# Performance work log

Hardware: AMD Instinct MI355X
Metric: run time of the kernel (lower is better)

## Reference

```python
import jax, jax.numpy as jnp
import numpy as np

N_NODES = 100000

def _gcn_norm(edge_index, num_nodes):
    # add self-loops, compute symmetric normalization coeffs per edge
    loops = jnp.arange(num_nodes, dtype=edge_index.dtype)
    src = jnp.concatenate([edge_index[0], loops])
    dst = jnp.concatenate([edge_index[1], loops])
    deg = jax.ops.segment_sum(jnp.ones_like(dst, dtype=jnp.float32), dst,
                              num_segments=num_nodes)
    dinv = jnp.where(deg > 0, jax.lax.rsqrt(deg), 0.0)
    norm = dinv[src] * dinv[dst]  # [E + N]
    return src, dst, norm

def _gcn_conv(x, W, b, src, dst, norm, num_nodes):
    h = x @ W                              # [N, out] transform first (PyG order)
    msg = h[src] * norm[:, None]           # gather + scale
    out = jax.ops.segment_sum(msg, dst, num_segments=num_nodes)  # scatter-add
    return out + b

def setup_inputs() -> dict:
    key = jax.random.key(0)
    k1, k2, k3, k4 = jax.random.split(key, 4)
    F_in, H, C = 128, 64, 40
    x = jax.random.normal(k1, (N_NODES, F_in), dtype=jnp.float32)
    edge_index = jax.random.randint(k2, (2, 1600000), 0, N_NODES, dtype=jnp.int64)
    W1 = jax.random.normal(k3, (F_in, H), dtype=jnp.float32) / np.sqrt(F_in)
    b1 = jnp.zeros((H,), dtype=jnp.float32)
    W2 = jax.random.normal(k4, (H, C), dtype=jnp.float32) / np.sqrt(H)
    b2 = jnp.zeros((C,), dtype=jnp.float32)
    return {"x": x, "edge_index": edge_index, "W1": W1, "b1": b1, "W2": W2, "b2": b2}

def reference(x, edge_index, W1, b1, W2, b2):
    num_nodes = x.shape[0]
    src, dst, norm = _gcn_norm(edge_index, num_nodes)
    h = _gcn_conv(x, W1, b1, src, dst, norm, num_nodes)
    h = jax.nn.relu(h)
    # dropout is identity in eval mode (training=False)
    h = _gcn_conv(h, W2, b2, src, dst, norm, num_nodes)
    return jax.nn.log_softmax(h, axis=1)
```

## Files before the change

kernel.cpp:

```cpp
#include <hip/hip_runtime.h>
#include <math.h>

#define NPB 256
#define BSH 8
#define MAXNB 400
#define BIN_CHUNK 8192
#define HIST_CHUNK 16384

typedef __attribute__((ext_vector_type(8))) short bf16x8;
typedef __attribute__((ext_vector_type(4))) float f32x4;
typedef __attribute__((ext_vector_type(2))) float f32x2;

__device__ __forceinline__ unsigned short f2bf(float f){
  unsigned int u = __float_as_uint(f);
  unsigned int r = (u + 0x7FFFu + ((u >> 16) & 1u)) >> 16;
  return (unsigned short)r;
}

__device__ __forceinline__ bf16x8 cvt8(float4 a, float4 b){
  union { unsigned u[4]; bf16x8 v; } r;
  asm("v_cvt_pk_bf16_f32 %0, %1, %2" : "=v"(r.u[0]) : "v"(a.x), "v"(a.y));
  asm("v_cvt_pk_bf16_f32 %0, %1, %2" : "=v"(r.u[1]) : "v"(a.z), "v"(a.w));
  asm("v_cvt_pk_bf16_f32 %0, %1, %2" : "=v"(r.u[2]) : "v"(b.x), "v"(b.y));
  asm("v_cvt_pk_bf16_f32 %0, %1, %2" : "=v"(r.u[3]) : "v"(b.z), "v"(b.w));
  return r.v;
}

__global__ void k_prep(const float* __restrict__ W1, const float* __restrict__ W2,
                       unsigned short* __restrict__ w1t, unsigned short* __restrict__ w2t,
                       int* __restrict__ bcnt, int NB){
  int t = threadIdx.x;
  if(blockIdx.x == 0){
    for(int i = t; i < 8192; i += 256){
      int k = i >> 6, f = i & 63;
      w1t[f*128 + k] = f2bf(W1[i]);
    }
  } else {
    for(int i = t; i < 3072; i += 256){
      int c = i >> 6, k = i & 63;
      w2t[c*64 + k] = (c < 40) ? f2bf(W2[k*40 + c]) : (unsigned short)0;
    }
    for(int i = t; i < NB; i += 256) bcnt[i] = 0;
  }
}


__global__ __launch_bounds__(256) void k_bhist(const int* __restrict__ dst, int E,
                                               int* __restrict__ bcnt, int NB){
  __shared__ int l[MAXNB];
  int t = threadIdx.x;
  int base = blockIdx.x*HIST_CHUNK;
  int end = base + HIST_CHUNK; if(end > E) end = E;
  for(int b = t; b < NB; b += 256) l[b] = 0;
  __syncthreads();
  for(int i = base + t; i < end; i += 256) atomicAdd(&l[dst[i] >> BSH], 1);
  __syncthreads();
  for(int b = t; b < NB; b += 256){ int c = l[b]; if(c) atomicAdd(&bcnt[b], c); }
}

__global__ void k_bscan(const int* __restrict__ bcnt, int* __restrict__ bofs,
                        int* __restrict__ bcur, int NB, int E){
  __shared__ int sh[1024];
  int t = threadIdx.x;
  int c0 = (2*t   < NB) ? bcnt[2*t]   : 0;
  int c1 = (2*t+1 < NB) ? bcnt[2*t+1] : 0;
  sh[t] = c0 + c1; __syncthreads();
  for(int off = 1; off < 1024; off <<= 1){
    int v = (t >= off) ? sh[t - off] : 0;
    __syncthreads();
    sh[t] += v;
    __syncthreads();
  }
  int pairEx = sh[t] - (c0 + c1);
  if(2*t   < NB){ bofs[2*t]   = pairEx;      bcur[2*t]   = pairEx; }
  if(2*t+1 < NB){ bofs[2*t+1] = pairEx + c0; bcur[2*t+1] = pairEx + c0; }
  if(t == 0) bofs[NB] = E;
}

__global__ __launch_bounds__(256) void k_binpass(const int* __restrict__ src,
                          const int* __restrict__ dst, int E,
                          int* __restrict__ bcur, unsigned int* __restrict__ binned, int NB){
  __shared__ int lcnt[MAXNB];
  __shared__ int lpos[MAXNB];
  int t = threadIdx.x;
  int base = blockIdx.x * BIN_CHUNK;
  int end = base + BIN_CHUNK; if(end > E) end = E;
  for(int b = t; b < NB; b += 256) lcnt[b] = 0;
  __syncthreads();
  for(int i = base + t; i < end; i += 256)
    atomicAdd(&lcnt[dst[i] >> BSH], 1);
  __syncthreads();
  for(int b = t; b < NB; b += 256){
    int c = lcnt[b];
    lpos[b] = c ? atomicAdd(&bcur[b], c) : 0;
  }
  __syncthreads();
  for(int i = base + t; i < end; i += 256){
    int d = dst[i];
    int b = d >> BSH;
    unsigned int rec = (unsigned int)src[i] | ((unsigned int)(d & (NPB-1)) << 17);
    int p = atomicAdd(&lpos[b], 1);
    binned[p] = rec;
  }
}

__global__ __launch_bounds__(256) void k_bscatter(const unsigned int* __restrict__ binned,
     const int* __restrict__ bofs, int* __restrict__ csr, int* __restrict__ row_ofs,
     float* __restrict__ dinv, int N, int E, int NB){
  __shared__ int lcnt[NPB];
  __shared__ int lofs[NPB];
  __shared__ int lcur[NPB];
  __shared__ int wsum[4];
  int b = blockIdx.x, t = threadIdx.x;
  int beg = bofs[b], end = bofs[b+1];
  lcnt[t] = 0;
  __syncthreads();
  for(int i = beg + t; i < end; i += 256) atomicAdd(&lcnt[binned[i] >> 17], 1);
  __syncthreads();
  int c = lcnt[t];
  int lane = t & 63, wid = t >> 6;
  int v = c;
  #pragma unroll
  for(int off = 1; off < 64; off <<= 1){
    int nv = __shfl_up(v, off, 64);
    if(lane >= off) v += nv;
  }
  if(lane == 63) wsum[wid] = v;
  __syncthreads();
  int wpre = 0;
  #pragma unroll
  for(int k2 = 0; k2 < 4; k2++) if(k2 < wid) wpre += wsum[k2];
  int ex = wpre + v - c;
  lofs[t] = beg + ex; lcur[t] = 0;
  int node = (b << BSH) + t;
  if(node < N){
    row_ofs[node] = beg + ex;
    dinv[node] = rsqrtf((float)(c + 1));
  }
  __syncthreads();
  for(int i = beg + t; i < end; i += 256){
    unsigned int rec = binned[i];
    int dl = rec >> 17;
    int pos = lofs[dl] + atomicAdd(&lcur[dl], 1);
    csr[pos] = (int)(rec & 0x1FFFFu);
  }
  if(b == NB-1 && t == 0) row_ofs[N] = E;
}

__global__ __launch_bounds__(256) void k_gemm1(const float* __restrict__ x,
                        const unsigned short* __restrict__ w1t,
                        const float* __restrict__ dinv, unsigned int* __restrict__ g1, int n){
  __shared__ unsigned short xs[128*136];
  __shared__ unsigned short wt[64*136];
  int tid = threadIdx.x;
  int nodeBase = blockIdx.x*128;
  for(int i = tid; i < 1024; i += 256){
    int f = i >> 4, seg = i & 15;
    *(uint4*)&wt[f*136 + seg*8] = *(const uint4*)&w1t[f*128 + seg*8];
  }
  {
    const float4* x4 = (const float4*)x;
    for(int i = tid; i < 2048; i += 256){
      int node = i >> 4, seg = i & 15;
      float4 va = make_float4(0.f,0.f,0.f,0.f), vb = va;
      if(nodeBase + node < n){
        va = x4[(size_t)(nodeBase + node)*32 + seg*2];
        vb = x4[(size_t)(nodeBase + node)*32 + seg*2 + 1];
      }
      *(bf16x8*)&xs[node*136 + seg*8] = cvt8(va, vb);
    }
  }
  __syncthreads();

  int w = tid >> 6, lane = tid & 63;
  int ml = lane & 15, q = lane >> 4;
  int n0 = nodeBase + w*32 + ml;
  int n1 = n0 + 16;
  bool vn0 = n0 < n, vn1 = n1 < n;

  f32x4 a00 = {0.f,0.f,0.f,0.f}, a01 = {0.f,0.f,0.f,0.f},
        a02 = {0.f,0.f,0.f,0.f}, a03 = {0.f,0.f,0.f,0.f};
  f32x4 a10 = {0.f,0.f,0.f,0.f}, a11 = {0.f,0.f,0.f,0.f},
        a12 = {0.f,0.f,0.f,0.f}, a13 = {0.f,0.f,0.f,0.f};
  const unsigned short* brow = &xs[(w*32 + ml)*136 + q*8];
  const unsigned short* arow = &wt[ml*136 + q*8];
  #pragma unroll
  for(int s = 0; s < 4; s++){
    bf16x8 bb0 = *(const bf16x8*)(brow +        s*32);
    bf16x8 bb1 = *(const bf16x8*)(brow + 2176 + s*32);
    bf16x8 a0 = *(const bf16x8*)(arow +    0 + s*32);
    bf16x8 a1 = *(const bf16x8*)(arow + 2176 + s*32);
    bf16x8 a2 = *(const bf16x8*)(arow + 4352 + s*32);
    bf16x8 a3 = *(const bf16x8*)(arow + 6528 + s*32);
    a00 = __builtin_amdgcn_mfma_f32_16x16x32_bf16(a0, bb0, a00, 0, 0, 0);
    a01 = __builtin_amdgcn_mfma_f32_16x16x32_bf16(a1, bb0, a01, 0, 0, 0);
    a02 = __builtin_amdgcn_mfma_f32_16x16x32_bf16(a2, bb0, a02, 0, 0, 0);
    a03 = __builtin_amdgcn_mfma_f32_16x16x32_bf16(a3, bb0, a03, 0, 0, 0);
    a10 = __builtin_amdgcn_mfma_f32_16x16x32_bf16(a0, bb1, a10, 0, 0, 0);
    a11 = __builtin_amdgcn_mfma_f32_16x16x32_bf16(a1, bb1, a11, 0, 0, 0);
    a12 = __builtin_amdgcn_mfma_f32_16x16x32_bf16(a2, bb1, a12, 0, 0, 0);
    a13 = __builtin_amdgcn_mfma_f32_16x16x32_bf16(a3, bb1, a13, 0, 0, 0);
  }
  if(vn0){
    float dv = dinv[n0];
    unsigned base16 = ((unsigned)n0 << 4) + q;
    int p;
    p = __builtin_amdgcn_cvt_pk_fp8_f32(a00[0]*dv, a00[1]*dv, 0, false);
    p = __builtin_amdgcn_cvt_pk_fp8_f32(a00[2]*dv, a00[3]*dv, p, true);
    g1[base16 +  0] = (unsigned)p;
    p = __builtin_amdgcn_cvt_pk_fp8_f32(a01[0]*dv, a01[1]*dv, 0, false);
    p = __builtin_amdgcn_cvt_pk_fp8_f32(a01[2]*dv, a01[3]*dv, p, true);
    g1[base16 +  4] = (unsigned)p;
    p = __builtin_amdgcn_cvt_pk_fp8_f32(a02[0]*dv, a02[1]*dv, 0, false);
    p = __builtin_amdgcn_cvt_pk_fp8_f32(a02[2]*dv, a02[3]*dv, p, true);
    g1[base16 +  8] = (unsigned)p;
    p = __builtin_amdgcn_cvt_pk_fp8_f32(a03[0]*dv, a03[1]*dv, 0, false);
    p = __builtin_amdgcn_cvt_pk_fp8_f32(a03[2]*dv, a03[3]*dv, p, true);
    g1[base16 + 12] = (unsigned)p;
  }
  if(vn1){
    float dv = dinv[n1];
    unsigned base16 = ((unsigned)n1 << 4) + q;
    int p;
    p = __builtin_amdgcn_cvt_pk_fp8_f32(a10[0]*dv, a10[1]*dv, 0, false);
    p = __builtin_amdgcn_cvt_pk_fp8_f32(a10[2]*dv, a10[3]*dv, p, true);
    g1[base16 +  0] = (unsigned)p;
    p = __builtin_amdgcn_cvt_pk_fp8_f32(a11[0]*dv, a11[1]*dv, 0, false);
    p = __builtin_amdgcn_cvt_pk_fp8_f32(a11[2]*dv, a11[3]*dv, p, true);
    g1[base16 +  4] = (unsigned)p;
    p = __builtin_amdgcn_cvt_pk_fp8_f32(a12[0]*dv, a12[1]*dv, 0, false);
    p = __builtin_amdgcn_cvt_pk_fp8_f32(a12[2]*dv, a12[3]*dv, p, true);
    g1[base16 +  8] = (unsigned)p;
    p = __builtin_amdgcn_cvt_pk_fp8_f32(a13[0]*dv, a13[1]*dv, 0, false);
    p = __builtin_amdgcn_cvt_pk_fp8_f32(a13[2]*dv, a13[3]*dv, p, true);
    g1[base16 + 12] = (unsigned)p;
  }
}

__global__ __launch_bounds__(256) void k_agg1(const unsigned* __restrict__ g1,
    const int* __restrict__ row_ofs, const int* __restrict__ csr,
    const float* __restrict__ dinv, const float* __restrict__ b1,
    unsigned short* __restrict__ u, int N){
  int t = threadIdx.x;
  int lane = t & 63;
  int f = lane & 15;
  int bq = (lane & 48) << 2;
  int node = blockIdx.x*16 + (t >> 4);
  if(node >= N) return;
  int beg = row_ofs[node], end = row_ofs[node+1];
  unsigned v = g1[((unsigned)node << 4) + f];
  f32x2 s01 = __builtin_amdgcn_cvt_pk_f32_fp8(v, false);
  f32x2 s23 = __builtin_amdgcn_cvt_pk_f32_fp8(v, true);
  for(int e = beg; e < end; e += 16){
    int rem = end - e; if(rem > 16) rem = 16;
    int idxv = (f < rem) ? csr[e + f] : 0;
    int j = 0;
    for(; j + 4 <= rem; j += 4){
      int r0 = __builtin_amdgcn_ds_bpermute(bq + ((j+0) << 2), idxv);
      int r1 = __builtin_amdgcn_ds_bpermute(bq + ((j+1) << 2), idxv);
      int r2 = __builtin_amdgcn_ds_bpermute(bq + ((j+2) << 2), idxv);
      int r3 = __builtin_amdgcn_ds_bpermute(bq + ((j+3) << 2), idxv);
      unsigned v0 = g1[((unsigned)r0 << 4) + f];
      unsigned v1 = g1[((unsigned)r1 << 4) + f];
      unsigned v2 = g1[((unsigned)r2 << 4) + f];
      unsigned v3 = g1[((unsigned)r3 << 4) + f];
      s01 += __builtin_amdgcn_cvt_pk_f32_fp8(v0, false);
      s23 += __builtin_amdgcn_cvt_pk_f32_fp8(v0, true);
      s01 += __builtin_amdgcn_cvt_pk_f32_fp8(v1, false);
      s23 += __builtin_amdgcn_cvt_pk_f32_fp8(v1, true);
      s01 += __builtin_amdgcn_cvt_pk_f32_fp8(v2, false);
      s23 += __builtin_amdgcn_cvt_pk_f32_fp8(v2, true);
      s01 += __builtin_amdgcn_cvt_pk_f32_fp8(v3, false);
      s23 += __builtin_amdgcn_cvt_pk_f32_fp8(v3, true);
    }
    for(; j < rem; j++){
      int r0 = __builtin_amdgcn_ds_bpermute(bq + (j << 2), idxv);
      unsigned v0 = g1[((unsigned)r0 << 4) + f];
      s01 += __builtin_amdgcn_cvt_pk_f32_fp8(v0, false);
      s23 += __builtin_amdgcn_cvt_pk_f32_fp8(v0, true);
    }
  }
  float dv = dinv[node];
  float4 bb = ((const float4*)b1)[f];
  float h0 = fmaxf(fmaf(dv, s01.x, bb.x), 0.f);
  float h1 = fmaxf(fmaf(dv, s01.y, bb.y), 0.f);
  float h2 = fmaxf(fmaf(dv, s23.x, bb.z), 0.f);
  float h3 = fmaxf(fmaf(dv, s23.y, bb.w), 0.f);
  unsigned p0 = (unsigned)f2bf(dv*h0) | ((unsigned)f2bf(dv*h1) << 16);
  unsigned p1 = (unsigned)f2bf(dv*h2) | ((unsigned)f2bf(dv*h3) << 16);
  ((uint2*)u)[((unsigned)node << 4) + f] = make_uint2(p0, p1);
}

__global__ __launch_bounds__(256) void k_gemm2(const unsigned short* __restrict__ u,
                        const unsigned short* __restrict__ w2t,
                        unsigned char* __restrict__ g2, int n){
  __shared__ unsigned short us[64*72];
  __shared__ unsigned short ws2[48*72];
  int t = threadIdx.x;
  int nodeBase = blockIdx.x*64;
  for(int i = t; i < 512; i += 256){
    int row = i >> 3, seg = i & 7;
    uint4 v = make_uint4(0,0,0,0);
    if(nodeBase + row < n) v = *(const uint4*)&u[(size_t)(nodeBase + row)*64 + seg*8];
    *(uint4*)&us[row*72 + seg*8] = v;
  }
  for(int i = t; i < 384; i += 256){
    int row = i >> 3, seg = i & 7;
    *(uint4*)&ws2[row*72 + seg*8] = *(const uint4*)&w2t[row*64 + seg*8];
  }
  __syncthreads();
  int w = t >> 6, lane = t & 63;
  int ml = lane & 15, q = lane >> 4;
  f32x4 acc0 = {0.f,0.f,0.f,0.f}, acc1 = {0.f,0.f,0.f,0.f}, acc2 = {0.f,0.f,0.f,0.f};
  const unsigned short* brow = &us[(w*16 + ml)*72 + q*8];
  const unsigned short* a0r = &ws2[ml*72 + q*8];
  #pragma unroll
  for(int s = 0; s < 2; s++){
    bf16x8 bb = *(const bf16x8*)(brow + s*32);
    bf16x8 a0 = *(const bf16x8*)(a0r +    0 + s*32);
    bf16x8 a1 = *(const bf16x8*)(a0r + 1152 + s*32);
    bf16x8 a2 = *(const bf16x8*)(a0r + 2304 + s*32);
    acc0 = __builtin_amdgcn_mfma_f32_16x16x32_bf16(a0, bb, acc0, 0, 0, 0);
    acc1 = __builtin_amdgcn_mfma_f32_16x16x32_bf16(a1, bb, acc1, 0, 0, 0);
    acc2 = __builtin_amdgcn_mfma_f32_16x16x32_bf16(a2, bb, acc2, 0, 0, 0);
  }
  int node = nodeBase + w*16 + ml;
  if(node < n){
    unsigned* gd = (unsigned*)g2;
    unsigned rb = (unsigned)node*10u + q;
    int p;
    p = __builtin_amdgcn_cvt_pk_fp8_f32(acc0[0], acc0[1], 0, false);
    p = __builtin_amdgcn_cvt_pk_fp8_f32(acc0[2], acc0[3], p, true);
    gd[rb + 0] = (unsigned)p;
    p = __builtin_amdgcn_cvt_pk_fp8_f32(acc1[0], acc1[1], 0, false);
    p = __builtin_amdgcn_cvt_pk_fp8_f32(acc1[2], acc1[3], p, true);
    gd[rb + 4] = (unsigned)p;
    if(q < 2){
      p = __builtin_amdgcn_cvt_pk_fp8_f32(acc2[0], acc2[1], 0, false);
      p = __builtin_amdgcn_cvt_pk_fp8_f32(acc2[2], acc2[3], p, true);
      gd[rb + 8] = (unsigned)p;
    }
  }
}

__global__ __launch_bounds__(256) void k_agg2(const unsigned char* __restrict__ g2,
     const int* __restrict__ row_ofs, const int* __restrict__ csr,
     const float* __restrict__ dinv, const float* __restrict__ b2,
     float* __restrict__ out, int N){
  int t = threadIdx.x;
  int lane = t & 63;
  int f = lane & 15;
  int fc = (f < 10) ? f : 0;
  int bq = (lane & 48) << 2;
  int node = blockIdx.x*16 + (t >> 4);
  if(node >= N) return;
  int beg = row_ofs[node], end = row_ofs[node+1];
  const unsigned* gd = (const unsigned*)g2;
  unsigned v = gd[(unsigned)node*10u + fc];
  f32x2 s01 = __builtin_amdgcn_cvt_pk_f32_fp8(v, false);
  f32x2 s23 = __builtin_amdgcn_cvt_pk_f32_fp8(v, true);
  for(int e = beg; e < end; e += 16){
    int rem = end - e; if(rem > 16) rem = 16;
    int idxv = (f < rem) ? csr[e + f] : 0;
    int j = 0;
    for(; j + 4 <= rem; j += 4){
      int r0 = __builtin_amdgcn_ds_bpermute(bq + ((j+0) << 2), idxv);
      int r1 = __builtin_amdgcn_ds_bpermute(bq + ((j+1) << 2), idxv);
      int r2 = __builtin_amdgcn_ds_bpermute(bq + ((j+2) << 2), idxv);
      int r3 = __builtin_amdgcn_ds_bpermute(bq + ((j+3) << 2), idxv);
      unsigned v0 = gd[(unsigned)r0*10u + fc];
      unsigned v1 = gd[(unsigned)r1*10u + fc];
      unsigned v2 = gd[(unsigned)r2*10u + fc];
      unsigned v3 = gd[(unsigned)r3*10u + fc];
      s01 += __builtin_amdgcn_cvt_pk_f32_fp8(v0, false);
      s23 += __builtin_amdgcn_cvt_pk_f32_fp8(v0, true);
      s01 += __builtin_amdgcn_cvt_pk_f32_fp8(v1, false);
      s23 += __builtin_amdgcn_cvt_pk_f32_fp8(v1, true);
      s01 += __builtin_amdgcn_cvt_pk_f32_fp8(v2, false);
      s23 += __builtin_amdgcn_cvt_pk_f32_fp8(v2, true);
      s01 += __builtin_amdgcn_cvt_pk_f32_fp8(v3, false);
      s23 += __builtin_amdgcn_cvt_pk_f32_fp8(v3, true);
    }
    for(; j < rem; j++){
      int r0 = __builtin_amdgcn_ds_bpermute(bq + (j << 2), idxv);
      unsigned v0 = gd[(unsigned)r0*10u + fc];
      s01 += __builtin_amdgcn_cvt_pk_f32_fp8(v0, false);
      s23 += __builtin_amdgcn_cvt_pk_f32_fp8(v0, true);
    }
  }
  float dv = dinv[node];
  float4 bb = ((const float4*)b2)[fc];
  float l0 = fmaf(dv, s01.x, bb.x);
  float l1 = fmaf(dv, s01.y, bb.y);
  float l2 = fmaf(dv, s23.x, bb.z);
  float l3 = fmaf(dv, s23.y, bb.w);
  bool valid = (f < 10);
  float m = valid ? fmaxf(fmaxf(l0,l1), fmaxf(l2,l3)) : -INFINITY;
  m = fmaxf(m, __shfl_xor(m,1,64)); m = fmaxf(m, __shfl_xor(m,2,64));
  m = fmaxf(m, __shfl_xor(m,4,64)); m = fmaxf(m, __shfl_xor(m,8,64));
  float ex = valid ? (expf(l0-m)+expf(l1-m)) + (expf(l2-m)+expf(l3-m)) : 0.f;
  ex += __shfl_xor(ex,1,64); ex += __shfl_xor(ex,2,64);
  ex += __shfl_xor(ex,4,64); ex += __shfl_xor(ex,8,64);
  float ll = logf(ex);
  if(valid){
    ((float4*)out)[(unsigned)node*10u + f] = make_float4(l0-m-ll, l1-m-ll, l2-m-ll, l3-m-ll);
  }
}


extern "C" void kernel_launch(void* const* d_in, const int* in_sizes, int n_in,
                              void* d_out, int out_size, void* d_ws, size_t ws_size,
                              hipStream_t stream){
  const float* x  = (const float*)d_in[0];
  const int*   ei = (const int*)  d_in[1];
  const float* W1 = (const float*)d_in[2];
  const float* b1 = (const float*)d_in[3];
  const float* W2 = (const float*)d_in[4];
  const float* b2 = (const float*)d_in[5];
  float* out = (float*)d_out;

  int N = in_sizes[0] / 128;
  int E = in_sizes[1] / 2;
  const int* src = ei;
  const int* dst = ei + E;
  int NB = (N + NPB - 1) >> BSH;

  char* w = (char*)d_ws;
  auto alloc = [&](size_t bytes) -> char* {
    char* p = w;
    w += (bytes + 511) & ~(size_t)511;
    return p;
  };
  int*   bcnt    = (int*)  alloc((size_t)NB*4);
  int*   bofs    = (int*)  alloc((size_t)(NB+1)*4);
  int*   bcur    = (int*)  alloc((size_t)NB*4);
  int*   row_ofs = (int*)  alloc((size_t)(N+1)*4);
  float* dinv    = (float*)alloc((size_t)N*4);
  unsigned int* binned = (unsigned int*)alloc((size_t)E*4);
  int*   csr     = (int*)  alloc((size_t)E*4);
  unsigned int*   g1 = (unsigned int*)  alloc((size_t)N*64);
  unsigned short* u  = (unsigned short*)alloc((size_t)N*64*2);
  unsigned char*  g2 = (unsigned char*) alloc((size_t)N*40);
  unsigned short* w1t = (unsigned short*)alloc((size_t)64*128*2);
  unsigned short* w2t = (unsigned short*)alloc((size_t)48*64*2);

  k_prep    <<<2, 256, 0, stream>>>(W1, W2, w1t, w2t, bcnt, NB);
  k_bhist   <<<(E+HIST_CHUNK-1)/HIST_CHUNK, 256, 0, stream>>>(dst, E, bcnt, NB);
  k_bscan   <<<1, 1024, 0, stream>>>(bcnt, bofs, bcur, NB, E);
  k_binpass <<<(E+BIN_CHUNK-1)/BIN_CHUNK, 256, 0, stream>>>(src, dst, E, bcur, binned, NB);
  k_bscatter<<<NB, 256, 0, stream>>>(binned, bofs, csr, row_ofs, dinv, N, E, NB);

  k_gemm1   <<<(N+127)/128, 256, 0, stream>>>(x, w1t, dinv, g1, N);
  k_agg1    <<<(N+15)/16, 256, 0, stream>>>(g1, row_ofs, csr, dinv, b1, u, N);
  k_gemm2   <<<(N+63)/64, 256, 0, stream>>>(u, w2t, g2, N);
  k_agg2    <<<(N+15)/16, 256, 0, stream>>>(g2, row_ofs, csr, dinv, b2, out, N);
}
```

Measured before the change: 232.3 us.

## Fuse layer-1 aggregation with layer-2 GEMM through shared memory

Merges the first-layer neighbor aggregation and the second-layer MFMA transform into one kernel. Each block aggregates 64 nodes (4 per 16-lane group, processed serially), writes the bf16 hidden rows straight into LDS, then runs the MFMA against W2. This removes the global write and re-read of the N×64 bf16 intermediate and one kernel launch. In exchange, the grid has 4x fewer blocks, each with more serial gather work, which may reduce latency hiding and worsen load balance on the irregular gathers.

After: 228.1 us. No clear change (-1.8%).

```diff
diff --git a/kernel.cpp b/kernel.cpp
--- a/kernel.cpp
+++ b/kernel.cpp
@@ -237,79 +237,76 @@
   }
 }
 
-__global__ __launch_bounds__(256) void k_agg1(const unsigned* __restrict__ g1,
+__global__ __launch_bounds__(256) void k_agg1g2(const unsigned* __restrict__ g1,
     const int* __restrict__ row_ofs, const int* __restrict__ csr,
     const float* __restrict__ dinv, const float* __restrict__ b1,
-    unsigned short* __restrict__ u, int N){
-  int t = threadIdx.x;
+    const unsigned short* __restrict__ w2t, unsigned char* __restrict__ g2, int n){
+  __shared__ unsigned short us[64*72];
+  __shared__ unsigned short ws2[48*72];
+  int t = threadIdx.x;
+  int nodeBase = blockIdx.x*64;
+  for(int i = t; i < 384; i += 256){
+    int row = i >> 3, seg = i & 7;
+    *(uint4*)&ws2[row*72 + seg*8] = *(const uint4*)&w2t[row*64 + seg*8];
+  }
   int lane = t & 63;
   int f = lane & 15;
   int bq = (lane & 48) << 2;
-  int node = blockIdx.x*16 + (t >> 4);
-  if(node >= N) return;
-  int beg = row_ofs[node], end = row_ofs[node+1];
-  unsigned v = g1[((unsigned)node << 4) + f];
-  f32x2 s01 = __builtin_amdgcn_cvt_pk_f32_fp8(v, false);
-  f32x2 s23 = __builtin_amdgcn_cvt_pk_f32_fp8(v, true);
-  for(int e = beg; e < end; e += 16){
-    int rem = end - e; if(rem > 16) rem = 16;
-    int idxv = (f < rem) ? csr[e + f] : 0;
-    int j = 0;
-    for(; j + 4 <= rem; j += 4){
-      int r0 = __builtin_amdgcn_ds_bpermute(bq + ((j+0) << 2), idxv);
-      int r1 = __builtin_amdgcn_ds_bpermute(bq + ((j+1) << 2), idxv);
-      int r2 = __builtin_amdgcn_ds_bpermute(bq + ((j+2) << 2), idxv);
-      int r3 = __builtin_amdgcn_ds_bpermute(bq + ((j+3) << 2), idxv);
-      unsigned v0 = g1[((unsigned)r0 << 4) + f];
-      unsigned v1 = g1[((unsigned)r1 << 4) + f];
-      unsigned v2 = g1[((unsigned)r2 << 4) + f];
-      unsigned v3 = g1[((unsigned)r3 << 4) + f];
-      s01 += __builtin_amdgcn_cvt_pk_f32_fp8(v0, false);
-      s23 += __builtin_amdgcn_cvt_pk_f32_fp8(v0, true);
-      s01 += __builtin_amdgcn_cvt_pk_f32_fp8(v1, false);
-      s23 += __builtin_amdgcn_cvt_pk_f32_fp8(v1, true);
-      s01 += __builtin_amdgcn_cvt_pk_f32_fp8(v2, false);
-      s23 += __builtin_amdgcn_cvt_pk_f32_fp8(v2, true);
-      s01 += __builtin_amdgcn_cvt_pk_f32_fp8(v3, false);
-      s23 += __builtin_amdgcn_cvt_pk_f32_fp8(v3, true);
-    }
-    for(; j < rem; j++){
-      int r0 = __builtin_amdgcn_ds_bpermute(bq + (j << 2), idxv);
-      unsigned v0 = g1[((unsigned)r0 << 4) + f];
-      s01 += __builtin_amdgcn_cvt_pk_f32_fp8(v0, false);
-      s23 += __builtin_amdgcn_cvt_pk_f32_fp8(v0, true);
-    }
-  }
-  float dv = dinv[node];
-  float4 bb = ((const float4*)b1)[f];
-  float h0 = fmaxf(fmaf(dv, s01.x, bb.x), 0.f);
-  float h1 = fmaxf(fmaf(dv, s01.y, bb.y), 0.f);
-  float h2 = fmaxf(fmaf(dv, s23.x, bb.z), 0.f);
-  float h3 = fmaxf(fmaf(dv, s23.y, bb.w), 0.f);
-  unsigned p0 = (unsigned)f2bf(dv*h0) | ((unsigned)f2bf(dv*h1) << 16);
-  unsigned p1 = (unsigned)f2bf(dv*h2) | ((unsigned)f2bf(dv*h3) << 16);
-  ((uint2*)u)[((unsigned)node << 4) + f] = make_uint2(p0, p1);
-}
-
-__global__ __launch_bounds__(256) void k_gemm2(const unsigned short* __restrict__ u,
-                        const unsigned short* __restrict__ w2t,
-                        unsigned char* __restrict__ g2, int n){
-  __shared__ unsigned short us[64*72];
-  __shared__ unsigned short ws2[48*72];
-  int t = threadIdx.x;
-  int nodeBase = blockIdx.x*64;
-  for(int i = t; i < 512; i += 256){
-    int row = i >> 3, seg = i & 7;
-    uint4 v = make_uint4(0,0,0,0);
-    if(nodeBase + row < n) v = *(const uint4*)&u[(size_t)(nodeBase + row)*64 + seg*8];
-    *(uint4*)&us[row*72 + seg*8] = v;
-  }
-  for(int i = t; i < 384; i += 256){
-    int row = i >> 3, seg = i & 7;
-    *(uint4*)&ws2[row*72 + seg*8] = *(const uint4*)&w2t[row*64 + seg*8];
-  }
-  __syncthreads();
-  int w = t >> 6, lane = t & 63;
+  int qg = t >> 4;
+  float4 bb1 = ((const float4*)b1)[f];
+  #pragma unroll 1
+  for(int i = 0; i < 4; i++){
+    int node = nodeBase + qg*4 + i;
+    int lrow = qg*4 + i;
+    if(node < n){
+      int beg = row_ofs[node], end = row_ofs[node+1];
+      unsigned v = g1[((unsigned)node << 4) + f];
+      f32x2 s01 = __builtin_amdgcn_cvt_pk_f32_fp8(v, false);
+      f32x2 s23 = __builtin_amdgcn_cvt_pk_f32_fp8(v, true);
+      for(int e = beg; e < end; e += 16){
+        int rem = end - e; if(rem > 16) rem = 16;
+        int idxv = (f < rem) ? csr[e + f] : 0;
+        int j = 0;
+        for(; j + 4 <= rem; j += 4){
+          int r0 = __builtin_amdgcn_ds_bpermute(bq + ((j+0) << 2), idxv);
+          int r1 = __builtin_amdgcn_ds_bpermute(bq + ((j+1) << 2), idxv);
+          int r2 = __builtin_amdgcn_ds_bpermute(bq + ((j+2) << 2), idxv);
+          int r3 = __builtin_amdgcn_ds_bpermute(bq + ((j+3) << 2), idxv);
+          unsigned v0 = g1[((unsigned)r0 << 4) + f];
+          unsigned v1 = g1[((unsigned)r1 << 4) + f];
+          unsigned v2 = g1[((unsigned)r2 << 4) + f];
+          unsigned v3 = g1[((unsigned)r3 << 4) + f];
+          s01 += __builtin_amdgcn_cvt_pk_f32_fp8(v0, false);
+          s23 += __builtin_amdgcn_cvt_pk_f32_fp8(v0, true);
+          s01 += __builtin_amdgcn_cvt_pk_f32_fp8(v1, false);
+          s23 += __builtin_amdgcn_cvt_pk_f32_fp8(v1, true);
+          s01 += __builtin_amdgcn_cvt_pk_f32_fp8(v2, false);
+          s23 += __builtin_amdgcn_cvt_pk_f32_fp8(v2, true);
+          s01 += __builtin_amdgcn_cvt_pk_f32_fp8(v3, false);
+          s23 += __builtin_amdgcn_cvt_pk_f32_fp8(v3, true);
+        }
+        for(; j < rem; j++){
+          int r0 = __builtin_amdgcn_ds_bpermute(bq + (j << 2), idxv);
+          unsigned v0 = g1[((unsigned)r0 << 4) + f];
+          s01 += __builtin_amdgcn_cvt_pk_f32_fp8(v0, false);
+          s23 += __builtin_amdgcn_cvt_pk_f32_fp8(v0, true);
+        }
+      }
+      float dv = dinv[node];
+      float h0 = fmaxf(fmaf(dv, s01.x, bb1.x), 0.f);
+      float h1 = fmaxf(fmaf(dv, s01.y, bb1.y), 0.f);
+      float h2 = fmaxf(fmaf(dv, s23.x, bb1.z), 0.f);
+      float h3 = fmaxf(fmaf(dv, s23.y, bb1.w), 0.f);
+      unsigned p0, p1;
+      asm("v_cvt_pk_bf16_f32 %0, %1, %2" : "=v"(p0) : "v"(dv*h0), "v"(dv*h1));
+      asm("v_cvt_pk_bf16_f32 %0, %1, %2" : "=v"(p1) : "v"(dv*h2), "v"(dv*h3));
+      *(uint2*)&us[lrow*72 + f*4] = make_uint2(p0, p1);
+    } else {
+      *(uint2*)&us[lrow*72 + f*4] = make_uint2(0u, 0u);
+    }
+  }
+  __syncthreads();
+  int w = t >> 6;
   int ml = lane & 15, q = lane >> 4;
   f32x4 acc0 = {0.f,0.f,0.f,0.f}, acc1 = {0.f,0.f,0.f,0.f}, acc2 = {0.f,0.f,0.f,0.f};
   const unsigned short* brow = &us[(w*16 + ml)*72 + q*8];
@@ -439,7 +436,6 @@
   unsigned int* binned = (unsigned int*)alloc((size_t)E*4);
   int*   csr     = (int*)  alloc((size_t)E*4);
   unsigned int*   g1 = (unsigned int*)  alloc((size_t)N*64);
-  unsigned short* u  = (unsigned short*)alloc((size_t)N*64*2);
   unsigned char*  g2 = (unsigned char*) alloc((size_t)N*40);
   unsigned short* w1t = (unsigned short*)alloc((size_t)64*128*2);
   unsigned short* w2t = (unsigned short*)alloc((size_t)48*64*2);
@@ -451,7 +447,6 @@
   k_bscatter<<<NB, 256, 0, stream>>>(binned, bofs, csr, row_ofs, dinv, N, E, NB);
 
   k_gemm1   <<<(N+127)/128, 256, 0, stream>>>(x, w1t, dinv, g1, N);
-  k_agg1    <<<(N+15)/16, 256, 0, stream>>>(g1, row_ofs, csr, dinv, b1, u, N);
-  k_gemm2   <<<(N+63)/64, 256, 0, stream>>>(u, w2t, g2, N);
+  k_agg1g2  <<<(N+63)/64, 256, 0, stream>>>(g1, row_ofs, csr, dinv, b1, w2t, g2, N);
   k_agg2    <<<(N+15)/16, 256, 0, stream>>>(g2, row_ofs, csr, dinv, b2, out, N);
 }
```
